# Optimization experiments

Hardware: AMD Instinct MI355X
Metric: run time of the kernel (lower is better)

The kernel has to match this reference:

```python
import jax, jax.numpy as jnp
import numpy as np

B, L, D = 64, 256, 768
LABELS = 200
REL_OFF = 256  # to_pos[k] = k + 256


def setup_inputs() -> dict:
    key = jax.random.key(0)
    ks = jax.random.split(key, 8)
    return {
        "sequence_output": jax.random.normal(ks[0], (B, L, D), dtype=jnp.float32),
        "pos_embedding": jax.random.normal(ks[1], (2 * REL_OFF + 1, D), dtype=jnp.float32) * 0.02,
        "class_embedding": jax.random.normal(ks[2], (LABELS + 1, D), dtype=jnp.float32) * 0.02,
        "W": jax.random.normal(ks[3], (LABELS, 3 * D), dtype=jnp.float32) * 0.02,
        "b": jnp.zeros((LABELS,), dtype=jnp.float32),
        "head_indexes": jax.random.randint(ks[4], (B, L), 0, L),
        "frame": jax.random.randint(ks[5], (B,), 0, LABELS + 1),
        "pos": jax.random.randint(ks[6], (B,), 0, L),
    }


def reference(sequence_output, pos_embedding, class_embedding, W, b, head_indexes, frame, pos):
    # per-batch gather of token rows: sequence_output[i] = sequence_output[i][head_indexes[i]]
    gathered = jnp.take_along_axis(sequence_output, head_indexes[:, :, None], axis=1)  # [B,L,D]

    j = jnp.arange(sequence_output.shape[1])  # [L]
    rel = j[None, :] - pos[:, None] + REL_OFF  # [B,L] in [0, 512]
    pe = pos_embedding[rel]  # [B,L,D]

    # frame embedding only at j == pos[i], else class_embedding[0]
    fe_hit = class_embedding[frame]  # [B,D]
    is_pos = (j[None, :] == pos[:, None])[:, :, None]  # [B,L,1]
    fe = jnp.where(is_pos, fe_hit[:, None, :], class_embedding[0][None, None, :])  # [B,L,D]

    feat = jnp.concatenate([gathered, pe, fe], axis=-1)  # [B,L,3D]
    # dropout is identity at inference; classifier linear
    return jnp.einsum("blf,cf->blc", feat, W) + b
```

## Files before the change

kernel.cpp:

```cpp
#include <hip/hip_runtime.h>
#include <stdint.h>


typedef __attribute__((ext_vector_type(8))) short short8;
typedef __attribute__((ext_vector_type(4))) float f32x4;

#define AS1 __attribute__((address_space(1)))
#define AS3 __attribute__((address_space(3)))

#define NSEQ_G 1572864
#define NPE_G  49248
#define NCE_G  19296
#define NW16_G 73728
#define SEQB_OFF 0
#define PEB_OFF  12582912
#define CEB_OFF  (PEB_OFF + 393984)
#define WP_OFF   (CEB_OFF + 154368)
#define WS_ELEMS (WP_OFF + 589824)
#define WS_NEED  ((size_t)WS_ELEMS * 2)
#define TILE_STRIDE 36864

__device__ __forceinline__ unsigned short f2bf(float f) {
    union { float f; unsigned int u; } v; v.f = f;
    unsigned int u = v.u;
    return (unsigned short)((u + 0x7fffu + ((u >> 16) & 1u)) >> 16);
}

__device__ __forceinline__ short8 pack8(f32x4 a, f32x4 b) {
    short8 r;
    r[0] = (short)f2bf(a.x); r[1] = (short)f2bf(a.y);
    r[2] = (short)f2bf(a.z); r[3] = (short)f2bf(a.w);
    r[4] = (short)f2bf(b.x); r[5] = (short)f2bf(b.y);
    r[6] = (short)f2bf(b.z); r[7] = (short)f2bf(b.w);
    return r;
}

__device__ __forceinline__ void dma16(const unsigned short* g, AS3 unsigned short* l) {
    __builtin_amdgcn_global_load_lds((AS1 const unsigned int*)g,
                                     (AS3 unsigned int*)l, 16, 0, 0);
}

__global__ void prep_kernel(const float* __restrict__ seq,
                            const float* __restrict__ pe,
                            const float* __restrict__ ce,
                            const float* __restrict__ W,
                            unsigned short* __restrict__ ws) {
    int g = blockIdx.x * 256 + threadIdx.x;
    if (g < NSEQ_G) {
        const float* p = seq + (size_t)g * 8;
        *(short8*)(ws + SEQB_OFF + (size_t)g * 8) =
            pack8(*(const f32x4*)p, *(const f32x4*)(p + 4));
        return;
    }
    g -= NSEQ_G;
    if (g < NPE_G) {
        const float* p = pe + (size_t)g * 8;
        *(short8*)(ws + PEB_OFF + (size_t)g * 8) =
            pack8(*(const f32x4*)p, *(const f32x4*)(p + 4));
        return;
    }
    g -= NPE_G;
    if (g < NCE_G) {
        const float* p = ce + (size_t)g * 8;
        *(short8*)(ws + CEB_OFF + (size_t)g * 8) =
            pack8(*(const f32x4*)p, *(const f32x4*)(p + 4));
        return;
    }
    g -= NCE_G;
    if (g < NW16_G) {
        int n   = g & 15;
        int kb8 = (g >> 4) % 288;
        int t   = g / (288 * 16);
        int row = t * 16 + n;
        int col = kb8 * 8;
        f32x4 a = {0.f, 0.f, 0.f, 0.f}, b = {0.f, 0.f, 0.f, 0.f};
        if (row < 200) {
            const float* p = W + (size_t)row * 2304 + col;
            a = *(const f32x4*)p;
            b = *(const f32x4*)(p + 4);
        }
        *(short8*)(ws + WP_OFF + (size_t)g * 8) = pack8(a, b);
    }
}

__global__ __launch_bounds__(512) void gemm5_kernel(
    const unsigned short* __restrict__ ws,
    const float* __restrict__ bias,
    const int*   __restrict__ head,
    const int*   __restrict__ frame,
    const int*   __restrict__ pos,
    float* __restrict__ out)
{
    __shared__ unsigned short lds[4096 + 8192];

    const unsigned short* seqb = ws + SEQB_OFF;
    const unsigned short* peb  = ws + PEB_OFF;
    const unsigned short* ceb  = ws + CEB_OFF;
    const unsigned short* Wp   = ws + WP_OFF;

    const int tid  = threadIdx.x;
    const int wave = tid >> 6;
    const int lane = tid & 63;
    const int n16  = lane & 15;
    const int quad = lane >> 4;

    const int mblk = blockIdx.x & 255;
    const int h    = blockIdx.x >> 8;

    const int i       = mblk >> 2;
    const int pos_i   = pos[i];
    const int frame_i = frame[i];

    const int smf = wave & 3;
    const int sks = wave >> 2;
    const int srow = mblk * 64 + smf * 16 + n16;
    const unsigned short* aSt[3];
    {
        const int sj   = srow & 255;
        const int shi  = head[srow];
        const int srel = sj - pos_i + 256;
        const int scls = (sj == pos_i) ? frame_i : 0;
        const int loff = sks * 32 + quad * 8;
        aSt[0] = seqb + ((size_t)i * 256 + (size_t)shi) * 768 + loff;
        aSt[1] = peb + (size_t)srel * 768 + loff;
        aSt[2] = ceb + (size_t)scls * 768 + loff;
    }
    AS3 unsigned short* aDst =
        (AS3 unsigned short*)lds + ((smf * 2 + sks) * 64 + lane) * 8;

    const unsigned short* bSt = Wp + (size_t)(h * 8 + wave) * TILE_STRIDE + lane * 8;
    AS3 unsigned short* bDst =
        (AS3 unsigned short*)lds + 4096 + wave * 1024 + lane * 8;

    const int p = wave & 1;
    const int q = wave >> 1;

    const unsigned short* aRd[2][2];
    const unsigned short* bRd[2][2];
#pragma unroll
    for (int f = 0; f < 2; ++f)
#pragma unroll
        for (int ks = 0; ks < 2; ++ks)
            aRd[f][ks] = lds + (((2 * p + f) * 2 + ks) * 64 + lane) * 8;
#pragma unroll
    for (int u = 0; u < 2; ++u)
#pragma unroll
        for (int ks = 0; ks < 2; ++ks)
            bRd[u][ks] = lds + 4096 + (q + 4 * u) * 1024 + ks * 512 + lane * 8;

    f32x4 acc[2][2];
#pragma unroll
    for (int u = 0; u < 2; ++u) {
        const int col = (h * 8 + q + 4 * u) * 16 + n16;
        const float bv = (col < 200) ? bias[col] : 0.0f;
        acc[0][u] = (f32x4){bv, bv, bv, bv};
        acc[1][u] = (f32x4){bv, bv, bv, bv};
    }

#pragma unroll
    for (int sg = 0; sg < 3; ++sg) {
        const unsigned short* aSrc = aSt[sg];
        const unsigned short* bSrc = bSt + (size_t)sg * 12288;
        for (int cc = 0; cc < 12; ++cc) {
            dma16(aSrc + cc * 64, aDst);
            dma16(bSrc + cc * 1024, bDst);
            dma16(bSrc + cc * 1024 + 512, bDst + 512);
            __syncthreads();
#pragma unroll
            for (int ks = 0; ks < 2; ++ks) {
                short8 a0 = *(const short8*)aRd[0][ks];
                short8 a1 = *(const short8*)aRd[1][ks];
#pragma unroll
                for (int u = 0; u < 2; ++u) {
                    short8 bf = *(const short8*)bRd[u][ks];
                    acc[0][u] = __builtin_amdgcn_mfma_f32_16x16x32_bf16(a0, bf, acc[0][u], 0, 0, 0);
                    acc[1][u] = __builtin_amdgcn_mfma_f32_16x16x32_bf16(a1, bf, acc[1][u], 0, 0, 0);
                }
            }
            __syncthreads();
        }
    }

#pragma unroll
    for (int f = 0; f < 2; ++f) {
        const int rbase = mblk * 64 + (2 * p + f) * 16 + quad * 4;
#pragma unroll
        for (int u = 0; u < 2; ++u) {
            const int col = (h * 8 + q + 4 * u) * 16 + n16;
            if (col < 200) {
#pragma unroll
                for (int r = 0; r < 4; ++r)
                    out[(size_t)(rbase + r) * 200 + col] = acc[f][u][r];
            }
        }
    }
}

__global__ __launch_bounds__(256) void gemm_fallback(
    const float* __restrict__ seq, const float* __restrict__ pe,
    const float* __restrict__ ce, const float* __restrict__ Wf,
    const float* __restrict__ bias, const int* __restrict__ head,
    const int* __restrict__ frame, const int* __restrict__ pos,
    float* __restrict__ out)
{
    const int tid  = threadIdx.x;
    const int wave = tid >> 6;
    const int lane = tid & 63;
    const int n16  = lane & 15;
    const int quad = lane >> 4;

    const int mrow  = blockIdx.x * 16 + n16;
    const int i     = mrow >> 8;
    const int j     = mrow & 255;
    const int pos_i = pos[i];
    const int hi    = head[mrow];
    const int rel   = j - pos_i + 256;
    const int cls   = (j == pos_i) ? frame[i] : 0;

    const float* segs[3];
    segs[0] = seq + ((size_t)i * 256 + (size_t)hi) * 768 + quad * 8;
    segs[1] = pe + (size_t)rel * 768 + quad * 8;
    segs[2] = ce + (size_t)cls * 768 + quad * 8;

    const int ntl = (wave == 0) ? 4 : 3;
    f32x4 acc[4];
#pragma unroll
    for (int u = 0; u < 4; ++u) {
        const int t = wave + 4 * u;
        const int col = t * 16 + n16;
        const float bv = (t < 13 && col < 200) ? bias[col] : 0.0f;
        acc[u] = (f32x4){bv, bv, bv, bv};
    }

    for (int s = 0; s < 3; ++s) {
        const float* ap = segs[s];
#pragma unroll 2
        for (int kk = 0; kk < 768; kk += 32) {
            short8 afr = pack8(*(const f32x4*)(ap + kk), *(const f32x4*)(ap + kk + 4));
#pragma unroll
            for (int u = 0; u < 4; ++u) {
                if (u < ntl) {
                    const int t = wave + 4 * u;
                    const int row = t * 16 + n16;
                    short8 bfr = {0, 0, 0, 0, 0, 0, 0, 0};
                    if (row < 200) {
                        const float* qp = Wf + (size_t)row * 2304 + s * 768 + kk + quad * 8;
                        bfr = pack8(*(const f32x4*)qp, *(const f32x4*)(qp + 4));
                    }
                    acc[u] = __builtin_amdgcn_mfma_f32_16x16x32_bf16(afr, bfr, acc[u], 0, 0, 0);
                }
            }
        }
    }

    const int rbase = blockIdx.x * 16 + quad * 4;
#pragma unroll
    for (int u = 0; u < 4; ++u) {
        const int t = wave + 4 * u;
        if (t < 13) {
            const int col = t * 16 + n16;
            if (col < 200) {
#pragma unroll
                for (int r = 0; r < 4; ++r)
                    out[(size_t)(rbase + r) * 200 + col] = acc[u][r];
            }
        }
    }
}

extern "C" void kernel_launch(void* const* d_in, const int* in_sizes, int n_in,
                              void* d_out, int out_size, void* d_ws, size_t ws_size,
                              hipStream_t stream) {
    const float* seq  = (const float*)d_in[0];
    const float* pe   = (const float*)d_in[1];
    const float* ce   = (const float*)d_in[2];
    const float* W    = (const float*)d_in[3];
    const float* bias = (const float*)d_in[4];
    const int* head   = (const int*)d_in[5];
    const int* frame  = (const int*)d_in[6];
    const int* pos    = (const int*)d_in[7];
    float* out = (float*)d_out;

    if (d_ws != nullptr && ws_size >= WS_NEED) {
        unsigned short* ws = (unsigned short*)d_ws;
        const int total_g = NSEQ_G + NPE_G + NCE_G + NW16_G;
        prep_kernel<<<(total_g + 255) / 256, 256, 0, stream>>>(seq, pe, ce, W, ws);
        gemm5_kernel<<<512, 512, 0, stream>>>(ws, bias, head, frame, pos, out);
    } else {
        gemm_fallback<<<1024, 256, 0, stream>>>(seq, pe, ce, W, bias, head,
                                                frame, pos, out);
    }
}
```

Baseline: 131.6 us.

## Double-buffer LDS staging and widen GEMM block to cover all output columns

```diff
diff --git a/kernel.cpp b/kernel.cpp
--- a/kernel.cpp
+++ b/kernel.cpp
@@ -19,6 +19,7 @@
 #define WS_ELEMS (WP_OFF + 589824)
 #define WS_NEED  ((size_t)WS_ELEMS * 2)
 #define TILE_STRIDE 36864
+#define BUFS 20480
 
 __device__ __forceinline__ unsigned short f2bf(float f) {
     union { float f; unsigned int u; } v; v.f = f;
@@ -83,7 +84,7 @@
     }
 }
 
-__global__ __launch_bounds__(512) void gemm5_kernel(
+__global__ __launch_bounds__(512) void gemm9_kernel(
     const unsigned short* __restrict__ ws,
     const float* __restrict__ bias,
     const int*   __restrict__ head,
@@ -91,7 +92,7 @@
     const int*   __restrict__ pos,
     float* __restrict__ out)
 {
-    __shared__ unsigned short lds[4096 + 8192];
+    __shared__ unsigned short lds[2 * BUFS];
 
     const unsigned short* seqb = ws + SEQB_OFF;
     const unsigned short* peb  = ws + PEB_OFF;
@@ -104,89 +105,93 @@
     const int n16  = lane & 15;
     const int quad = lane >> 4;
 
-    const int mblk = blockIdx.x & 255;
-    const int h    = blockIdx.x >> 8;
-
+    const int mblk = blockIdx.x;
     const int i       = mblk >> 2;
     const int pos_i   = pos[i];
     const int frame_i = frame[i];
 
-    const int smf = wave & 3;
-    const int sks = wave >> 2;
+    const int smf = wave >> 1;
+    const int sks = wave & 1;
     const int srow = mblk * 64 + smf * 16 + n16;
-    const unsigned short* aSt[3];
+    const unsigned short *aSt0, *aSt1, *aSt2;
     {
         const int sj   = srow & 255;
         const int shi  = head[srow];
         const int srel = sj - pos_i + 256;
         const int scls = (sj == pos_i) ? frame_i : 0;
         const int loff = sks * 32 + quad * 8;
-        aSt[0] = seqb + ((size_t)i * 256 + (size_t)shi) * 768 + loff;
-        aSt[1] = peb + (size_t)srel * 768 + loff;
-        aSt[2] = ceb + (size_t)scls * 768 + loff;
-    }
-    AS3 unsigned short* aDst =
-        (AS3 unsigned short*)lds + ((smf * 2 + sks) * 64 + lane) * 8;
-
-    const unsigned short* bSt = Wp + (size_t)(h * 8 + wave) * TILE_STRIDE + lane * 8;
-    AS3 unsigned short* bDst =
-        (AS3 unsigned short*)lds + 4096 + wave * 1024 + lane * 8;
+        aSt0 = seqb + ((size_t)i * 256 + (size_t)shi) * 768 + loff;
+        aSt1 = peb + (size_t)srel * 768 + loff;
+        aSt2 = ceb + (size_t)scls * 768 + loff;
+    }
+    const unsigned short* bSt0 = Wp + (size_t)(2 * wave) * TILE_STRIDE + lane * 8;
+    const unsigned short* bSt1 = bSt0 + TILE_STRIDE;
+
+    AS3 unsigned short* ldsw = (AS3 unsigned short*)lds;
+    const int aDstOff = (wave * 64 + lane) * 8;
+    const int bDstOff = 4096 + wave * 2048 + lane * 8;
 
     const int p = wave & 1;
     const int q = wave >> 1;
 
-    const unsigned short* aRd[2][2];
-    const unsigned short* bRd[2][2];
-#pragma unroll
-    for (int f = 0; f < 2; ++f)
-#pragma unroll
-        for (int ks = 0; ks < 2; ++ks)
-            aRd[f][ks] = lds + (((2 * p + f) * 2 + ks) * 64 + lane) * 8;
-#pragma unroll
-    for (int u = 0; u < 2; ++u)
-#pragma unroll
-        for (int ks = 0; ks < 2; ++ks)
-            bRd[u][ks] = lds + 4096 + (q + 4 * u) * 1024 + ks * 512 + lane * 8;
-
-    f32x4 acc[2][2];
-#pragma unroll
-    for (int u = 0; u < 2; ++u) {
-        const int col = (h * 8 + q + 4 * u) * 16 + n16;
+    f32x4 acc[2][4];
+#pragma unroll
+    for (int u = 0; u < 4; ++u) {
+        const int col = (q + 4 * u) * 16 + n16;
         const float bv = (col < 200) ? bias[col] : 0.0f;
         acc[0][u] = (f32x4){bv, bv, bv, bv};
         acc[1][u] = (f32x4){bv, bv, bv, bv};
     }
 
-#pragma unroll
-    for (int sg = 0; sg < 3; ++sg) {
-        const unsigned short* aSrc = aSt[sg];
-        const unsigned short* bSrc = bSt + (size_t)sg * 12288;
-        for (int cc = 0; cc < 12; ++cc) {
-            dma16(aSrc + cc * 64, aDst);
-            dma16(bSrc + cc * 1024, bDst);
-            dma16(bSrc + cc * 1024 + 512, bDst + 512);
-            __syncthreads();
-#pragma unroll
-            for (int ks = 0; ks < 2; ++ks) {
-                short8 a0 = *(const short8*)aRd[0][ks];
-                short8 a1 = *(const short8*)aRd[1][ks];
-#pragma unroll
-                for (int u = 0; u < 2; ++u) {
-                    short8 bf = *(const short8*)bRd[u][ks];
-                    acc[0][u] = __builtin_amdgcn_mfma_f32_16x16x32_bf16(a0, bf, acc[0][u], 0, 0, 0);
-                    acc[1][u] = __builtin_amdgcn_mfma_f32_16x16x32_bf16(a1, bf, acc[1][u], 0, 0, 0);
-                }
-            }
-            __syncthreads();
-        }
-    }
+    const int aRd0 = ((2 * p + 0) * 2) * 512 + lane * 8;
+    const int aRd1 = ((2 * p + 1) * 2) * 512 + lane * 8;
+    const int bRdB = 4096 + q * 1024 + quad * 128 + n16 * 8;
+
+    auto stage = [&](int c, int b) {
+        const unsigned short* ap;
+        int cc;
+        if (c < 12)      { ap = aSt0; cc = c; }
+        else if (c < 24) { ap = aSt1; cc = c - 12; }
+        else             { ap = aSt2; cc = c - 24; }
+        AS3 unsigned short* base = ldsw + b * BUFS;
+        dma16(ap + cc * 64, base + aDstOff);
+        const int co = c * 1024;
+        dma16(bSt0 + co,       base + bDstOff);
+        dma16(bSt0 + co + 512, base + bDstOff + 512);
+        dma16(bSt1 + co,       base + bDstOff + 1024);
+        dma16(bSt1 + co + 512, base + bDstOff + 1536);
+    };
+
+    auto compute = [&](int c) {
+        const unsigned short* base = lds + (c & 1) * BUFS;
+#pragma unroll
+        for (int ks = 0; ks < 2; ++ks) {
+            short8 a0 = *(const short8*)(base + aRd0 + ks * 512);
+            short8 a1 = *(const short8*)(base + aRd1 + ks * 512);
+#pragma unroll
+            for (int u = 0; u < 4; ++u) {
+                short8 bf = *(const short8*)(base + bRdB + u * 4096 + ks * 512);
+                acc[0][u] = __builtin_amdgcn_mfma_f32_16x16x32_bf16(a0, bf, acc[0][u], 0, 0, 0);
+                acc[1][u] = __builtin_amdgcn_mfma_f32_16x16x32_bf16(a1, bf, acc[1][u], 0, 0, 0);
+            }
+        }
+    };
+
+    stage(0, 0);
+    __syncthreads();
+    for (int c = 0; c < 35; ++c) {
+        stage(c + 1, (c + 1) & 1);
+        compute(c);
+        __syncthreads();
+    }
+    compute(35);
 
 #pragma unroll
     for (int f = 0; f < 2; ++f) {
         const int rbase = mblk * 64 + (2 * p + f) * 16 + quad * 4;
 #pragma unroll
-        for (int u = 0; u < 2; ++u) {
-            const int col = (h * 8 + q + 4 * u) * 16 + n16;
+        for (int u = 0; u < 4; ++u) {
+            const int col = (q + 4 * u) * 16 + n16;
             if (col < 200) {
 #pragma unroll
                 for (int r = 0; r < 4; ++r)
@@ -285,7 +290,7 @@
         unsigned short* ws = (unsigned short*)d_ws;
         const int total_g = NSEQ_G + NPE_G + NCE_G + NW16_G;
         prep_kernel<<<(total_g + 255) / 256, 256, 0, stream>>>(seq, pe, ce, W, ws);
-        gemm5_kernel<<<512, 512, 0, stream>>>(ws, bias, head, frame, pos, out);
+        gemm9_kernel<<<256, 512, 0, stream>>>(ws, bias, head, frame, pos, out);
     } else {
         gemm_fallback<<<1024, 256, 0, stream>>>(seq, pe, ce, W, bias, head,
                                                 frame, pos, out);
```

Result: slower. 134.5 us (+2.2%).

## Switch GEMM to 32x32x16 MFMA with 2-wave blocks and 32-row W tiles

Applied to the files above, without the earlier changes.

```diff
diff --git a/kernel.cpp b/kernel.cpp
--- a/kernel.cpp
+++ b/kernel.cpp
@@ -4,6 +4,7 @@
 
 typedef __attribute__((ext_vector_type(8))) short short8;
 typedef __attribute__((ext_vector_type(4))) float f32x4;
+typedef __attribute__((ext_vector_type(16))) float f32x16;
 
 #define AS1 __attribute__((address_space(1)))
 #define AS3 __attribute__((address_space(3)))
@@ -11,14 +12,14 @@
 #define NSEQ_G 1572864
 #define NPE_G  49248
 #define NCE_G  19296
-#define NW16_G 73728
+#define NW32_G 73728
 #define SEQB_OFF 0
 #define PEB_OFF  12582912
 #define CEB_OFF  (PEB_OFF + 393984)
 #define WP_OFF   (CEB_OFF + 154368)
 #define WS_ELEMS (WP_OFF + 589824)
 #define WS_NEED  ((size_t)WS_ELEMS * 2)
-#define TILE_STRIDE 36864
+#define T32_STRIDE 73728
 
 __device__ __forceinline__ unsigned short f2bf(float f) {
     union { float f; unsigned int u; } v; v.f = f;
@@ -67,12 +68,12 @@
         return;
     }
     g -= NCE_G;
-    if (g < NW16_G) {
-        int n   = g & 15;
-        int kb8 = (g >> 4) % 288;
-        int t   = g / (288 * 16);
-        int row = t * 16 + n;
-        int col = kb8 * 8;
+    if (g < NW32_G) {
+        int n  = g & 31;
+        int k8 = (g >> 5) % 288;
+        int t  = g / (288 * 32);
+        int row = t * 32 + n;
+        int col = k8 * 8;
         f32x4 a = {0.f, 0.f, 0.f, 0.f}, b = {0.f, 0.f, 0.f, 0.f};
         if (row < 200) {
             const float* p = W + (size_t)row * 2304 + col;
@@ -83,7 +84,7 @@
     }
 }
 
-__global__ __launch_bounds__(512) void gemm5_kernel(
+__global__ __launch_bounds__(128) void gemm10_kernel(
     const unsigned short* __restrict__ ws,
     const float* __restrict__ bias,
     const int*   __restrict__ head,
@@ -91,7 +92,8 @@
     const int*   __restrict__ pos,
     float* __restrict__ out)
 {
-    __shared__ unsigned short lds[4096 + 8192];
+    __shared__ unsigned short ldsA[4096];
+    __shared__ unsigned short ldsB[8192];
 
     const unsigned short* seqb = ws + SEQB_OFF;
     const unsigned short* peb  = ws + PEB_OFF;
@@ -101,96 +103,88 @@
     const int tid  = threadIdx.x;
     const int wave = tid >> 6;
     const int lane = tid & 63;
-    const int n16  = lane & 15;
-    const int quad = lane >> 4;
+    const int n32  = lane & 31;
+    const int half = lane >> 5;
 
     const int mblk = blockIdx.x & 255;
-    const int h    = blockIdx.x >> 8;
+    const int nh   = blockIdx.x >> 8;
 
     const int i       = mblk >> 2;
     const int pos_i   = pos[i];
     const int frame_i = frame[i];
 
-    const int smf = wave & 3;
-    const int sks = wave >> 2;
-    const int srow = mblk * 64 + smf * 16 + n16;
-    const unsigned short* aSt[3];
+    const int arow = mblk * 64 + wave * 32 + n32;
+    const unsigned short *aSeg[3];
     {
-        const int sj   = srow & 255;
-        const int shi  = head[srow];
-        const int srel = sj - pos_i + 256;
-        const int scls = (sj == pos_i) ? frame_i : 0;
-        const int loff = sks * 32 + quad * 8;
-        aSt[0] = seqb + ((size_t)i * 256 + (size_t)shi) * 768 + loff;
-        aSt[1] = peb + (size_t)srel * 768 + loff;
-        aSt[2] = ceb + (size_t)scls * 768 + loff;
-    }
-    AS3 unsigned short* aDst =
-        (AS3 unsigned short*)lds + ((smf * 2 + sks) * 64 + lane) * 8;
-
-    const unsigned short* bSt = Wp + (size_t)(h * 8 + wave) * TILE_STRIDE + lane * 8;
-    AS3 unsigned short* bDst =
-        (AS3 unsigned short*)lds + 4096 + wave * 1024 + lane * 8;
-
-    const int p = wave & 1;
-    const int q = wave >> 1;
-
-    const unsigned short* aRd[2][2];
-    const unsigned short* bRd[2][2];
-#pragma unroll
-    for (int f = 0; f < 2; ++f)
-#pragma unroll
-        for (int ks = 0; ks < 2; ++ks)
-            aRd[f][ks] = lds + (((2 * p + f) * 2 + ks) * 64 + lane) * 8;
-#pragma unroll
-    for (int u = 0; u < 2; ++u)
-#pragma unroll
-        for (int ks = 0; ks < 2; ++ks)
-            bRd[u][ks] = lds + 4096 + (q + 4 * u) * 1024 + ks * 512 + lane * 8;
-
-    f32x4 acc[2][2];
-#pragma unroll
-    for (int u = 0; u < 2; ++u) {
-        const int col = (h * 8 + q + 4 * u) * 16 + n16;
+        const int aj   = arow & 255;
+        const int ahi  = head[arow];
+        const int arel = aj - pos_i + 256;
+        const int acls = (aj == pos_i) ? frame_i : 0;
+        const int loff = half * 8;
+        aSeg[0] = seqb + ((size_t)i * 256 + (size_t)ahi) * 768 + loff;
+        aSeg[1] = peb + (size_t)arel * 768 + loff;
+        aSeg[2] = ceb + (size_t)acls * 768 + loff;
+    }
+    AS3 unsigned short* aD = (AS3 unsigned short*)ldsA + wave * 2048 + lane * 8;
+
+    const unsigned short* bSt0 = Wp + (size_t)(nh * 4 + 2 * wave) * T32_STRIDE + lane * 8;
+    const unsigned short* bSt1 = bSt0 + T32_STRIDE;
+    AS3 unsigned short* bD = (AS3 unsigned short*)ldsB + (2 * wave) * 2048 + lane * 8;
+
+    f32x16 acc[2][2];
+#pragma unroll
+    for (int ni = 0; ni < 2; ++ni) {
+        const int col = nh * 128 + (2 * wave + ni) * 32 + n32;
         const float bv = (col < 200) ? bias[col] : 0.0f;
-        acc[0][u] = (f32x4){bv, bv, bv, bv};
-        acc[1][u] = (f32x4){bv, bv, bv, bv};
-    }
+#pragma unroll
+        for (int f = 0; f < 2; ++f)
+#pragma unroll
+            for (int r = 0; r < 16; ++r) acc[f][ni][r] = bv;
+    }
+
+    const int bRd0 = (2 * wave) * 2048 + lane * 8;
 
 #pragma unroll
     for (int sg = 0; sg < 3; ++sg) {
-        const unsigned short* aSrc = aSt[sg];
-        const unsigned short* bSrc = bSt + (size_t)sg * 12288;
+        const unsigned short* aSrc = aSeg[sg];
         for (int cc = 0; cc < 12; ++cc) {
-            dma16(aSrc + cc * 64, aDst);
-            dma16(bSrc + cc * 1024, bDst);
-            dma16(bSrc + cc * 1024 + 512, bDst + 512);
+            const int c = sg * 12 + cc;
+#pragma unroll
+            for (int kb = 0; kb < 4; ++kb)
+                dma16(aSrc + cc * 64 + kb * 16, aD + kb * 512);
+#pragma unroll
+            for (int r = 0; r < 4; ++r) {
+                dma16(bSt0 + (size_t)c * 2048 + r * 512, bD + r * 512);
+                dma16(bSt1 + (size_t)c * 2048 + r * 512, bD + 2048 + r * 512);
+            }
             __syncthreads();
 #pragma unroll
-            for (int ks = 0; ks < 2; ++ks) {
-                short8 a0 = *(const short8*)aRd[0][ks];
-                short8 a1 = *(const short8*)aRd[1][ks];
-#pragma unroll
-                for (int u = 0; u < 2; ++u) {
-                    short8 bf = *(const short8*)bRd[u][ks];
-                    acc[0][u] = __builtin_amdgcn_mfma_f32_16x16x32_bf16(a0, bf, acc[0][u], 0, 0, 0);
-                    acc[1][u] = __builtin_amdgcn_mfma_f32_16x16x32_bf16(a1, bf, acc[1][u], 0, 0, 0);
+            for (int kb = 0; kb < 4; ++kb) {
+                short8 a0 = *(const short8*)(ldsA + kb * 512 + lane * 8);
+                short8 a1 = *(const short8*)(ldsA + 2048 + kb * 512 + lane * 8);
+                short8 b0 = *(const short8*)(ldsB + bRd0 + kb * 512);
+                short8 b1 = *(const short8*)(ldsB + bRd0 + 2048 + kb * 512);
+                acc[0][0] = __builtin_amdgcn_mfma_f32_32x32x16_bf16(a0, b0, acc[0][0], 0, 0, 0);
+                acc[1][0] = __builtin_amdgcn_mfma_f32_32x32x16_bf16(a1, b0, acc[1][0], 0, 0, 0);
+                acc[0][1] = __builtin_amdgcn_mfma_f32_32x32x16_bf16(a0, b1, acc[0][1], 0, 0, 0);
+                acc[1][1] = __builtin_amdgcn_mfma_f32_32x32x16_bf16(a1, b1, acc[1][1], 0, 0, 0);
+            }
+            __syncthreads();
+        }
+    }
+
+#pragma unroll
+    for (int f = 0; f < 2; ++f) {
+        const int rb = mblk * 64 + f * 32 + 4 * half;
+#pragma unroll
+        for (int ni = 0; ni < 2; ++ni) {
+            const int col = nh * 128 + (2 * wave + ni) * 32 + n32;
+            if (col < 200) {
+#pragma unroll
+                for (int r = 0; r < 16; ++r) {
+                    const int row = rb + (r & 3) + 8 * (r >> 2);
+                    out[(size_t)row * 200 + col] = acc[f][ni][r];
                 }
-            }
-            __syncthreads();
-        }
-    }
-
-#pragma unroll
-    for (int f = 0; f < 2; ++f) {
-        const int rbase = mblk * 64 + (2 * p + f) * 16 + quad * 4;
-#pragma unroll
-        for (int u = 0; u < 2; ++u) {
-            const int col = (h * 8 + q + 4 * u) * 16 + n16;
-            if (col < 200) {
-#pragma unroll
-                for (int r = 0; r < 4; ++r)
-                    out[(size_t)(rbase + r) * 200 + col] = acc[f][u][r];
             }
         }
     }
@@ -283,9 +277,9 @@
 
     if (d_ws != nullptr && ws_size >= WS_NEED) {
         unsigned short* ws = (unsigned short*)d_ws;
-        const int total_g = NSEQ_G + NPE_G + NCE_G + NW16_G;
+        const int total_g = NSEQ_G + NPE_G + NCE_G + NW32_G;
         prep_kernel<<<(total_g + 255) / 256, 256, 0, stream>>>(seq, pe, ce, W, ws);
-        gemm5_kernel<<<512, 512, 0, stream>>>(ws, bias, head, frame, pos, out);
+        gemm10_kernel<<<512, 128, 0, stream>>>(ws, bias, head, frame, pos, out);
     } else {
         gemm_fallback<<<1024, 256, 0, stream>>>(seq, pe, ce, W, bias, head,
                                                 frame, pos, out);
```

Result: slower. 137.6 us (+4.6%).
